# Optimization experiments

Hardware: AMD Instinct MI355X
Metric: run time of the kernel (lower is better)

Reference implementation:

```python
import jax, jax.numpy as jnp
import numpy as np

NUM_CLASSES = 80
FOCAL_ALPHA = 0.25
FOCAL_GAMMA = 2.0
HUBER_SIGMA = 3.0
REG_MEAN = 0.0
REG_STD = 0.2
IMG_H = 800.0
IMG_W = 800.0
B, A, M = 4, 100000, 32


def setup_inputs() -> dict:
    key = jax.random.key(0)
    k1, k2, k3, k4, k5, k6, k7 = jax.random.split(key, 7)
    classification = jax.random.uniform(k1, (B, A, NUM_CLASSES), dtype=jnp.float32)
    regression = jax.random.normal(k2, (B, A, 4), dtype=jnp.float32)
    # plausible anchors: centers inside image, sizes 16..256
    cx = jax.random.uniform(k3, (A,), minval=0.0, maxval=IMG_W)
    cy = jax.random.uniform(k4, (A,), minval=0.0, maxval=IMG_H)
    s = jax.random.uniform(k5, (A, 2), minval=16.0, maxval=256.0)
    anchors = jnp.stack([cx - s[:, 0] / 2, cy - s[:, 1] / 2,
                         cx + s[:, 0] / 2, cy + s[:, 1] / 2], axis=1).astype(jnp.float32)
    # annotations: [B, M, 5] = x1,y1,x2,y2,class
    xy = jax.random.uniform(k6, (B, M, 2), minval=0.0, maxval=650.0)
    wh = jax.random.uniform(k7, (B, M, 2), minval=30.0, maxval=150.0)
    cls = jax.random.randint(jax.random.fold_in(key, 9), (B, M, 1), 0, NUM_CLASSES).astype(jnp.float32)
    annotations = jnp.concatenate([xy, xy + wh, cls], axis=-1)
    return {"classification": classification, "regression": regression,
            "anchors": anchors, "annotations": annotations}


def _pairwise_iou(anchors, boxes):
    # anchors [A,4], boxes [M,4] -> [A,M]
    ix1 = jnp.maximum(anchors[:, None, 0], boxes[None, :, 0])
    iy1 = jnp.maximum(anchors[:, None, 1], boxes[None, :, 1])
    ix2 = jnp.minimum(anchors[:, None, 2], boxes[None, :, 2])
    iy2 = jnp.minimum(anchors[:, None, 3], boxes[None, :, 3])
    inter = jnp.clip(ix2 - ix1, 0.0) * jnp.clip(iy2 - iy1, 0.0)
    area_a = (anchors[:, 2] - anchors[:, 0]) * (anchors[:, 3] - anchors[:, 1])
    area_b = (boxes[:, 2] - boxes[:, 0]) * (boxes[:, 3] - boxes[:, 1])
    union = area_a[:, None] + area_b[None, :] - inter
    return inter / jnp.maximum(union, 1e-8)


def _targets(anchors, annotations):
    # per-image anchor assignment, vmapped over batch
    def per_image(ann):
        boxes = ann[:, :4]
        cls = ann[:, 4].astype(jnp.int32)
        ious = _pairwise_iou(anchors, boxes)          # [A,M]
        best = jnp.argmax(ious, axis=1)               # [A]
        best_iou = jnp.max(ious, axis=1)
        pos = best_iou >= 0.5
        ign = (best_iou > 0.4) & (~pos)
        states = jnp.where(pos, 1.0, jnp.where(ign, -1.0, 0.0))
        cx = (anchors[:, 0] + anchors[:, 2]) * 0.5
        cy = (anchors[:, 1] + anchors[:, 3]) * 0.5
        inside = (cx >= 0) & (cx < IMG_W) & (cy >= 0) & (cy < IMG_H)
        states = jnp.where(inside, states, -1.0)
        labels = jax.nn.one_hot(cls[best], NUM_CLASSES, dtype=jnp.float32) * pos[:, None]
        ab = boxes[best]                              # assigned gt boxes [A,4]
        aw = anchors[:, 2] - anchors[:, 0]
        ah = anchors[:, 3] - anchors[:, 1]
        t = jnp.stack([(ab[:, 0] - anchors[:, 0]) / aw,
                       (ab[:, 1] - anchors[:, 1]) / ah,
                       (ab[:, 2] - anchors[:, 2]) / aw,
                       (ab[:, 3] - anchors[:, 3]) / ah], axis=1)
        t = (t - REG_MEAN) / REG_STD
        return labels, t, states
    return jax.vmap(per_image)(annotations)


def reference(classification, regression, anchors, annotations):
    labels, reg_t, states = _targets(anchors, annotations)   # [B,A,K],[B,A,4],[B,A]
    num_pos = jnp.maximum(jnp.sum((states == 1.0).astype(jnp.float32)), 1.0)
    # focal loss over non-ignored anchors
    valid = (states != -1.0)[..., None].astype(jnp.float32)
    p = jnp.clip(classification, 1e-4, 1.0 - 1e-4)
    bce = -(labels * jnp.log(p) + (1.0 - labels) * jnp.log1p(-p))
    alpha_f = jnp.where(labels == 1.0, FOCAL_ALPHA, 1.0 - FOCAL_ALPHA)
    focal_w = alpha_f * jnp.where(labels == 1.0, 1.0 - p, p) ** FOCAL_GAMMA
    cls_loss = jnp.sum(focal_w * bce * valid) / num_pos
    # smooth L1 over positive anchors
    pos_m = (states == 1.0)[..., None].astype(jnp.float32)
    s2 = HUBER_SIGMA ** 2
    d = jnp.abs(regression - reg_t)
    l1 = jnp.where(d < 1.0 / s2, 0.5 * s2 * d * d, d - 0.5 / s2)
    reg_loss = jnp.sum(l1 * pos_m) / num_pos
    return cls_loss + reg_loss
```

## Files before the change

kernel.cpp:

```cpp
#include <hip/hip_runtime.h>

#define BB 4
#define AA 100000
#define MM 32
#define NC 80
#define GX 391
#define NBLK (GX * BB)
#define FB 3125
#define FT (FB * 256)
#define N4 (BB * AA * (NC/4))
#define LN2 0.69314718055994530942f


__device__ __forceinline__ float hw_log2(float x) {
#if defined(__has_builtin)
#if __has_builtin(__builtin_amdgcn_logf)
    return __builtin_amdgcn_logf(x);
#else
    return __log2f(x);
#endif
#else
    return __log2f(x);
#endif
}

__global__ __launch_bounds__(256) void codes_kernel(
    const float* __restrict__ anchors,
    const float* __restrict__ annotations,
    const float* __restrict__ regression,
    float* __restrict__ reg_part,
    unsigned* __restrict__ pos_part,
    signed char* __restrict__ codes)
{
    __shared__ float ann[MM * 5];
    const int b = blockIdx.y;
    const int tid = threadIdx.x;
    if (tid < MM * 5) ann[tid] = annotations[b * MM * 5 + tid];
    __syncthreads();

    const int a = blockIdx.x * 256 + tid;
    float reg_sum = 0.0f;
    int pos_cnt = 0;

    if (a < AA) {
        const float4 an = ((const float4*)anchors)[a];
        const float ax1 = an.x, ay1 = an.y, ax2 = an.z, ay2 = an.w;
        const float area_a = __fmul_rn(__fsub_rn(ax2, ax1), __fsub_rn(ay2, ay1));

        float best_iou = -1.0f;
        int best = 0;
        #pragma unroll
        for (int j = 0; j < MM; ++j) {
            const float bx1 = ann[j * 5 + 0];
            const float by1 = ann[j * 5 + 1];
            const float bx2 = ann[j * 5 + 2];
            const float by2 = ann[j * 5 + 3];
            const float ix1 = fmaxf(ax1, bx1);
            const float iy1 = fmaxf(ay1, by1);
            const float ix2 = fminf(ax2, bx2);
            const float iy2 = fminf(ay2, by2);
            const float iw = fmaxf(__fsub_rn(ix2, ix1), 0.0f);
            const float ih = fmaxf(__fsub_rn(iy2, iy1), 0.0f);
            const float inter = __fmul_rn(iw, ih);
            const float area_b = __fmul_rn(__fsub_rn(bx2, bx1), __fsub_rn(by2, by1));
            const float uni = __fsub_rn(__fadd_rn(area_a, area_b), inter);
            const float iou = __fdiv_rn(inter, fmaxf(uni, 1e-8f));
            if (iou > best_iou) { best_iou = iou; best = j; }
        }

        const bool pos = best_iou >= 0.5f;
        const bool ign = (best_iou > 0.4f) && !pos;
        const float cx = (ax1 + ax2) * 0.5f;
        const float cy = (ay1 + ay2) * 0.5f;
        const bool inside = (cx >= 0.0f) && (cx < 800.0f) && (cy >= 0.0f) && (cy < 800.0f);

        int code = -2;
        if (inside && !ign) code = pos ? (int)ann[best * 5 + 4] : -1;
        codes[b * AA + a] = (signed char)code;

        if (pos && inside) {
            pos_cnt = 1;
            const float aw = ax2 - ax1;
            const float ah = ay2 - ay1;
            const float bx1 = ann[best * 5 + 0];
            const float by1 = ann[best * 5 + 1];
            const float bx2 = ann[best * 5 + 2];
            const float by2 = ann[best * 5 + 3];
            float t[4];
            t[0] = ((bx1 - ax1) / aw) / 0.2f;
            t[1] = ((by1 - ay1) / ah) / 0.2f;
            t[2] = ((bx2 - ax2) / aw) / 0.2f;
            t[3] = ((by2 - ay2) / ah) / 0.2f;
            const float* rg = regression + (((size_t)b * AA + a) * 4);
            #pragma unroll
            for (int k = 0; k < 4; ++k) {
                const float d = fabsf(rg[k] - t[k]);
                reg_sum += (d < (1.0f / 9.0f)) ? (4.5f * d * d) : (d - (0.5f / 9.0f));
            }
        }
    }

    #pragma unroll
    for (int off = 32; off > 0; off >>= 1) {
        reg_sum += __shfl_down(reg_sum, off);
        pos_cnt += __shfl_down(pos_cnt, off);
    }
    __shared__ float wr[4];
    __shared__ int   wp[4];
    const int wave = tid >> 6, lane = tid & 63;
    if (lane == 0) { wr[wave] = reg_sum; wp[wave] = pos_cnt; }
    __syncthreads();
    if (tid == 0) {
        const int idx = b * GX + blockIdx.x;
        reg_part[idx] = wr[0] + wr[1] + wr[2] + wr[3];
        pos_part[idx] = (unsigned)(wp[0] + wp[1] + wp[2] + wp[3]);
    }
}

__global__ __launch_bounds__(256) void focal_kernel(
    const float4* __restrict__ cls4,
    const signed char* __restrict__ codes,
    float* __restrict__ cls_part)
{
    const int t0 = blockIdx.x * 256 + threadIdx.x;
    float csum2 = 0.0f;
    float pcor2 = 0.0f;

    #pragma unroll
    for (int half = 0; half < 2; ++half) {
        float4 v[5];
        int    cd[5];
        #pragma unroll
        for (int k = 0; k < 5; ++k) {
            const int i = t0 + (half * 5 + k) * FT;
            v[k]  = cls4[i];
            cd[k] = codes[i / 20];
        }
        __builtin_amdgcn_sched_barrier(0);
        #pragma unroll
        for (int k = 0; k < 5; ++k) {
            const int i = t0 + (half * 5 + k) * FT;
            const int s = i / 20;
            const int colb = (i - s * 20) * 4;
            const int c = cd[k];

            const float p0 = fminf(fmaxf(v[k].x, 1e-4f), 0.9999f);
            const float p1 = fminf(fmaxf(v[k].y, 1e-4f), 0.9999f);
            const float p2 = fminf(fmaxf(v[k].z, 1e-4f), 0.9999f);
            const float p3 = fminf(fmaxf(v[k].w, 1e-4f), 0.9999f);
            const float l0 = hw_log2(1.0f - p0);
            const float l1 = hw_log2(1.0f - p1);
            const float l2 = hw_log2(1.0f - p2);
            const float l3 = hw_log2(1.0f - p3);
            float sub = -(p0 * p0 * l0);
            sub -= p1 * p1 * l1;
            sub -= p2 * p2 * l2;
            sub -= p3 * p3 * l3;
            csum2 += (c != -2) ? sub : 0.0f;

            const unsigned rel = (unsigned)(c - colb);
            if (rel < 4u) {
                const float p  = (rel & 2u) ? ((rel & 1u) ? p3 : p2) : ((rel & 1u) ? p1 : p0);
                const float ln = (rel & 2u) ? ((rel & 1u) ? l3 : l2) : ((rel & 1u) ? l1 : l0);
                const float onem = 1.0f - p;
                pcor2 -= onem * onem * hw_log2(p);
                csum2 += p * p * ln;
            }
        }
    }

    float csum = LN2 * (0.75f * csum2 + 0.25f * pcor2);

    #pragma unroll
    for (int off = 32; off > 0; off >>= 1) csum += __shfl_down(csum, off);
    __shared__ float wc[4];
    const int wave = threadIdx.x >> 6, lane = threadIdx.x & 63;
    if (lane == 0) wc[wave] = csum;
    __syncthreads();
    if (threadIdx.x == 0) cls_part[blockIdx.x] = wc[0] + wc[1] + wc[2] + wc[3];
}

__global__ __launch_bounds__(256) void finalize_kernel(
    const float* __restrict__ reg_part,
    const unsigned* __restrict__ pos_part,
    const float* __restrict__ cls_part,
    float* __restrict__ out)
{
    float cs = 0.0f, rs = 0.0f;
    unsigned pc = 0;
    for (int i = threadIdx.x; i < FB; i += 256) cs += cls_part[i];
    for (int i = threadIdx.x; i < NBLK; i += 256) { rs += reg_part[i]; pc += pos_part[i]; }
    #pragma unroll
    for (int off = 32; off > 0; off >>= 1) {
        cs += __shfl_down(cs, off);
        rs += __shfl_down(rs, off);
        pc += __shfl_down(pc, off);
    }
    __shared__ float wc[4], wr[4];
    __shared__ unsigned wp[4];
    const int wave = threadIdx.x >> 6, lane = threadIdx.x & 63;
    if (lane == 0) { wc[wave] = cs; wr[wave] = rs; wp[wave] = pc; }
    __syncthreads();
    if (threadIdx.x == 0) {
        const float csum = wc[0] + wc[1] + wc[2] + wc[3];
        const float rsum = wr[0] + wr[1] + wr[2] + wr[3];
        const float np = fmaxf((float)(wp[0] + wp[1] + wp[2] + wp[3]), 1.0f);
        out[0] = (csum + rsum) / np;
    }
}

extern "C" void kernel_launch(void* const* d_in, const int* in_sizes, int n_in,
                              void* d_out, int out_size, void* d_ws, size_t ws_size,
                              hipStream_t stream)
{
    const float* classification = (const float*)d_in[0];
    const float* regression     = (const float*)d_in[1];
    const float* anchors        = (const float*)d_in[2];
    const float* annotations    = (const float*)d_in[3];
    float* out = (float*)d_out;

    float*       reg_part = (float*)d_ws;
    unsigned*    pos_part = (unsigned*)d_ws + NBLK;
    float*       cls_part = (float*)d_ws + 2 * NBLK;
    signed char* codes    = (signed char*)d_ws + 65536;

    dim3 gA(GX, BB);
    codes_kernel<<<gA, 256, 0, stream>>>(anchors, annotations, regression,
                                         reg_part, pos_part, codes);
    focal_kernel<<<FB, 256, 0, stream>>>((const float4*)classification, codes, cls_part);
    finalize_kernel<<<1, 256, 0, stream>>>(reg_part, pos_part, cls_part, out);
}
```

Before: 210.2 us.

## Compute unconditional negative focal term first and correct per-anchor in targets kernel

The focal kernel now sums the negative focal term over every element without reading per-anchor codes. The targets kernel then subtracts that term for anchors outside the image or ignored, and swaps the negative term for the positive one at each positive anchor's class. This removes the codes buffer and its byte-wise gathers, and lets the big streaming pass run independently of anchor assignment. The cost is extra reads of full 80-class rows for excluded anchors, which are uncoalesced per-thread row loads, plus a subtraction that may lose some accuracy.

```diff
diff --git a/kernel.cpp b/kernel.cpp
--- a/kernel.cpp
+++ b/kernel.cpp
@@ -24,13 +24,24 @@
 #endif
 }
 
-__global__ __launch_bounds__(256) void codes_kernel(
+__device__ __forceinline__ float clampp(float p) {
+    return fminf(fmaxf(p, 1e-4f), 0.9999f);
+}
+__device__ __forceinline__ float fneg(float p) {
+    return 0.75f * p * p * (-LN2 * hw_log2(1.0f - p));
+}
+__device__ __forceinline__ float fpos(float p) {
+    const float q = 1.0f - p;
+    return 0.25f * q * q * (-LN2 * hw_log2(p));
+}
+
+__global__ __launch_bounds__(256) void targets_kernel(
     const float* __restrict__ anchors,
     const float* __restrict__ annotations,
     const float* __restrict__ regression,
+    const float* __restrict__ cls,
     float* __restrict__ reg_part,
-    unsigned* __restrict__ pos_part,
-    signed char* __restrict__ codes)
+    unsigned* __restrict__ pos_part)
 {
     __shared__ float ann[MM * 5];
     const int b = blockIdx.y;
@@ -39,7 +50,7 @@
     __syncthreads();
 
     const int a = blockIdx.x * 256 + tid;
-    float reg_sum = 0.0f;
+    float acc = 0.0f;
     int pos_cnt = 0;
 
     if (a < AA) {
@@ -76,7 +87,6 @@
 
         int code = -2;
         if (inside && !ign) code = pos ? (int)ann[best * 5 + 4] : -1;
-        codes[b * AA + a] = (signed char)code;
 
         if (pos && inside) {
             pos_cnt = 1;
@@ -95,20 +105,33 @@
             #pragma unroll
             for (int k = 0; k < 4; ++k) {
                 const float d = fabsf(rg[k] - t[k]);
-                reg_sum += (d < (1.0f / 9.0f)) ? (4.5f * d * d) : (d - (0.5f / 9.0f));
+                acc += (d < (1.0f / 9.0f)) ? (4.5f * d * d) : (d - (0.5f / 9.0f));
             }
         }
+
+        if (code == -2) {
+            const float4* c4 = (const float4*)cls + ((size_t)b * AA + a) * 20;
+            #pragma unroll 4
+            for (int k = 0; k < 20; ++k) {
+                const float4 v = c4[k];
+                acc -= fneg(clampp(v.x)) + fneg(clampp(v.y))
+                     + fneg(clampp(v.z)) + fneg(clampp(v.w));
+            }
+        } else if (code >= 0) {
+            const float p = clampp(cls[((size_t)b * AA + a) * NC + code]);
+            acc += fpos(p) - fneg(p);
+        }
     }
 
     #pragma unroll
     for (int off = 32; off > 0; off >>= 1) {
-        reg_sum += __shfl_down(reg_sum, off);
+        acc     += __shfl_down(acc, off);
         pos_cnt += __shfl_down(pos_cnt, off);
     }
     __shared__ float wr[4];
     __shared__ int   wp[4];
     const int wave = tid >> 6, lane = tid & 63;
-    if (lane == 0) { wr[wave] = reg_sum; wp[wave] = pos_cnt; }
+    if (lane == 0) { wr[wave] = acc; wp[wave] = pos_cnt; }
     __syncthreads();
     if (tid == 0) {
         const int idx = b * GX + blockIdx.x;
@@ -119,57 +142,27 @@
 
 __global__ __launch_bounds__(256) void focal_kernel(
     const float4* __restrict__ cls4,
-    const signed char* __restrict__ codes,
     float* __restrict__ cls_part)
 {
     const int t0 = blockIdx.x * 256 + threadIdx.x;
-    float csum2 = 0.0f;
-    float pcor2 = 0.0f;
-
-    #pragma unroll
-    for (int half = 0; half < 2; ++half) {
-        float4 v[5];
-        int    cd[5];
-        #pragma unroll
-        for (int k = 0; k < 5; ++k) {
-            const int i = t0 + (half * 5 + k) * FT;
-            v[k]  = cls4[i];
-            cd[k] = codes[i / 20];
-        }
-        __builtin_amdgcn_sched_barrier(0);
-        #pragma unroll
-        for (int k = 0; k < 5; ++k) {
-            const int i = t0 + (half * 5 + k) * FT;
-            const int s = i / 20;
-            const int colb = (i - s * 20) * 4;
-            const int c = cd[k];
-
-            const float p0 = fminf(fmaxf(v[k].x, 1e-4f), 0.9999f);
-            const float p1 = fminf(fmaxf(v[k].y, 1e-4f), 0.9999f);
-            const float p2 = fminf(fmaxf(v[k].z, 1e-4f), 0.9999f);
-            const float p3 = fminf(fmaxf(v[k].w, 1e-4f), 0.9999f);
-            const float l0 = hw_log2(1.0f - p0);
-            const float l1 = hw_log2(1.0f - p1);
-            const float l2 = hw_log2(1.0f - p2);
-            const float l3 = hw_log2(1.0f - p3);
-            float sub = -(p0 * p0 * l0);
-            sub -= p1 * p1 * l1;
-            sub -= p2 * p2 * l2;
-            sub -= p3 * p3 * l3;
-            csum2 += (c != -2) ? sub : 0.0f;
-
-            const unsigned rel = (unsigned)(c - colb);
-            if (rel < 4u) {
-                const float p  = (rel & 2u) ? ((rel & 1u) ? p3 : p2) : ((rel & 1u) ? p1 : p0);
-                const float ln = (rel & 2u) ? ((rel & 1u) ? l3 : l2) : ((rel & 1u) ? l1 : l0);
-                const float onem = 1.0f - p;
-                pcor2 -= onem * onem * hw_log2(p);
-                csum2 += p * p * ln;
-            }
-        }
-    }
-
-    float csum = LN2 * (0.75f * csum2 + 0.25f * pcor2);
+    float4 v[10];
+    #pragma unroll
+    for (int k = 0; k < 10; ++k) v[k] = cls4[t0 + k * FT];
+    __builtin_amdgcn_sched_barrier(0);
+
+    float s0 = 0.0f, s1 = 0.0f, s2 = 0.0f, s3 = 0.0f;
+    #pragma unroll
+    for (int k = 0; k < 10; ++k) {
+        const float p0 = clampp(v[k].x);
+        const float p1 = clampp(v[k].y);
+        const float p2 = clampp(v[k].z);
+        const float p3 = clampp(v[k].w);
+        s0 -= p0 * p0 * hw_log2(1.0f - p0);
+        s1 -= p1 * p1 * hw_log2(1.0f - p1);
+        s2 -= p2 * p2 * hw_log2(1.0f - p2);
+        s3 -= p3 * p3 * hw_log2(1.0f - p3);
+    }
+    float csum = (0.75f * LN2) * ((s0 + s1) + (s2 + s3));
 
     #pragma unroll
     for (int off = 32; off > 0; off >>= 1) csum += __shfl_down(csum, off);
@@ -219,14 +212,13 @@
     const float* annotations    = (const float*)d_in[3];
     float* out = (float*)d_out;
 
-    float*       reg_part = (float*)d_ws;
-    unsigned*    pos_part = (unsigned*)d_ws + NBLK;
-    float*       cls_part = (float*)d_ws + 2 * NBLK;
-    signed char* codes    = (signed char*)d_ws + 65536;
-
+    float*    reg_part = (float*)d_ws;
+    unsigned* pos_part = (unsigned*)d_ws + NBLK;
+    float*    cls_part = (float*)d_ws + 2 * NBLK;
+
+    focal_kernel<<<FB, 256, 0, stream>>>((const float4*)classification, cls_part);
     dim3 gA(GX, BB);
-    codes_kernel<<<gA, 256, 0, stream>>>(anchors, annotations, regression,
-                                         reg_part, pos_part, codes);
-    focal_kernel<<<FB, 256, 0, stream>>>((const float4*)classification, codes, cls_part);
+    targets_kernel<<<gA, 256, 0, stream>>>(anchors, annotations, regression,
+                                           classification, reg_part, pos_part);
     finalize_kernel<<<1, 256, 0, stream>>>(reg_part, pos_part, cls_part, out);
 }
```

Result: slower. 216.8 us (+3.2%).
